# Optimization experiments

Measured on AMD Instinct MI355X. Metric: run time of the kernel, lower is better.

The kernel has to match this reference:

```python
import jax, jax.numpy as jnp
import numpy as np

N_T, N_C, N_I = 200000, 100000, 100000  # target / card / ip node counts
E = 300000                               # edges per relation
D, H, OUT = 128, 128, 2                  # embedding_size=in_size, hidden_size, out_size
# etype order: 0 card->target, 1 target->card, 2 ip->target, 3 target->ip


def setup_inputs() -> dict:
    key = jax.random.key(0)
    ks = jax.random.split(key, 14)
    return {
        "x_target": jax.random.normal(ks[0], (N_T, D), jnp.float32),
        "x_card": jax.random.normal(ks[1], (N_C, D), jnp.float32),
        "x_ip": jax.random.normal(ks[2], (N_I, D), jnp.float32),
        "w1": jax.random.normal(ks[3], (4, D, H), jnp.float32) / np.sqrt(D).astype(np.float32),
        "b1": jnp.zeros((4, H), jnp.float32),
        "w2": jax.random.normal(ks[4], (4, H, H), jnp.float32) / np.sqrt(H).astype(np.float32),
        "b2": jnp.zeros((4, H), jnp.float32),
        "w_out": jax.random.normal(ks[5], (H, OUT), jnp.float32) / np.sqrt(H).astype(np.float32),
        "b_out": jnp.zeros((OUT,), jnp.float32),
        "src0": jax.random.randint(ks[6], (E,), 0, N_C, jnp.int32),
        "dst0": jax.random.randint(ks[7], (E,), 0, N_T, jnp.int32),
        "src1": jax.random.randint(ks[8], (E,), 0, N_T, jnp.int32),
        "dst1": jax.random.randint(ks[9], (E,), 0, N_C, jnp.int32),
        "src2": jax.random.randint(ks[10], (E,), 0, N_I, jnp.int32),
        "dst2": jax.random.randint(ks[11], (E,), 0, N_T, jnp.int32),
        "src3": jax.random.randint(ks[12], (E,), 0, N_T, jnp.int32),
        "dst3": jax.random.randint(ks[13], (E,), 0, N_I, jnp.int32),
    }


def _mean_agg(msgs, dst, num_dst):
    # copy_u + mean reduce: segment-sum of gathered messages / in-degree (0 if no edges)
    s = jax.ops.segment_sum(msgs, dst, num_segments=num_dst)
    deg = jax.ops.segment_sum(jnp.ones((msgs.shape[0],), msgs.dtype), dst, num_segments=num_dst)
    return s / jnp.maximum(deg, 1.0)[:, None]


def _hetero_layer(feats, W, B, edges):
    # per-etype Linear on src feats, copy_u/mean per relation, sum across relations per dsttype
    out = {}
    for i, (src, dst, st, dt, nd) in enumerate(edges):
        Wh = feats[st] @ W[i] + B[i]          # [N_src, H] dense GEMM per etype
        agg = _mean_agg(Wh[src], dst, nd)      # gather + segment-mean (irregular)
        out[dt] = agg if dt not in out else out[dt] + agg
    return out


def reference(x_target, x_card, x_ip, w1, b1, w2, b2, w_out, b_out,
              src0, dst0, src1, dst1, src2, dst2, src3, dst3):
    edges = [
        (src0, dst0, "card", "target", N_T),
        (src1, dst1, "target", "card", N_C),
        (src2, dst2, "ip", "target", N_T),
        (src3, dst3, "target", "ip", N_I),
    ]
    h = {"target": x_target, "card": x_card, "ip": x_ip}
    h = _hetero_layer(h, w1, b1, edges)
    h = {k: jax.nn.leaky_relu(v) for k, v in h.items()}  # applied before layer i>0
    h = _hetero_layer(h, w2, b2, edges)
    logits = h["target"] @ w_out + b_out
    return jax.nn.softmax(logits, axis=-1)
```

## Files before the change

### kernel.cpp

```cpp
#include <hip/hip_runtime.h>


#define NT 200000
#define NCARD 100000
#define NIP 100000
#define NE 300000

typedef __attribute__((ext_vector_type(8))) short s8v;
typedef __attribute__((ext_vector_type(4))) float f4v;

__device__ __forceinline__ unsigned short f2b(float f) {
  unsigned u = __float_as_uint(f);
  u = (u + 0x7fff + ((u >> 16) & 1)) >> 16;
  return (unsigned short)u;
}


__global__ void hist4_k(const int* __restrict__ d1, const int* __restrict__ d3,
                        const int* __restrict__ d0, const int* __restrict__ d2,
                        int* __restrict__ g1, int* __restrict__ g3,
                        int* __restrict__ g0, int* __restrict__ g2) {
  int t = blockIdx.x * 256 + threadIdx.x;
  if (t < NE) atomicAdd(&g1[d1[t]], 1);
  else if (t < 2 * NE) atomicAdd(&g3[d3[t - NE]], 1);
  else if (t < 3 * NE) atomicAdd(&g0[d0[t - 2 * NE]], 1);
  else if (t < 4 * NE) atomicAdd(&g2[d2[t - 3 * NE]], 1);
}


__global__ void scan1f_k(const int* __restrict__ deg1, int* __restrict__ off1,
                         int* __restrict__ bs1, int nb1, int N1,
                         const int* __restrict__ deg3, int* __restrict__ off3,
                         int* __restrict__ bs3, int N3) {
  __shared__ int s[256];
  int bid = blockIdx.x;
  const int* deg; int* off; int* bsum; int N; int lb;
  if (bid < nb1) { deg = deg1; off = off1; bsum = bs1; N = N1; lb = bid; }
  else { deg = deg3; off = off3; bsum = bs3; N = N3; lb = bid - nb1; }
  int tid = threadIdx.x;
  int i = lb * 256 + tid;
  int v = (i < N) ? deg[i] : 0;
  s[tid] = v;
  __syncthreads();
  for (int o = 1; o < 256; o <<= 1) {
    int t = (tid >= o) ? s[tid - o] : 0;
    __syncthreads();
    s[tid] += t;
    __syncthreads();
  }
  if (i < N) off[i] = s[tid] - v;
  if (tid == 255) bsum[lb] = s[255];
}

__global__ void scan2f_k(int* __restrict__ bs1, int nb1, int* __restrict__ bs3, int nb3) {
  __shared__ int s[1024];
  int* bs = blockIdx.x == 0 ? bs1 : bs3;
  int nb = blockIdx.x == 0 ? nb1 : nb3;
  int t = threadIdx.x;
  int v = (t < nb) ? bs[t] : 0;
  s[t] = v;
  __syncthreads();
  for (int o = 1; o < 1024; o <<= 1) {
    int u = (t >= o) ? s[t - o] : 0;
    __syncthreads();
    s[t] += u;
    __syncthreads();
  }
  if (t < nb) bs[t] = s[t] - v;
}

__global__ void scan3f_k(int* __restrict__ off1, const int* __restrict__ bs1,
                         int* __restrict__ cur1, int nb1, int N1,
                         int* __restrict__ off3, const int* __restrict__ bs3,
                         int* __restrict__ cur3, int N3) {
  int bid = blockIdx.x;
  int* off; const int* bsum; int* cur; int N; int lb;
  if (bid < nb1) { off = off1; bsum = bs1; cur = cur1; N = N1; lb = bid; }
  else { off = off3; bsum = bs3; cur = cur3; N = N3; lb = bid - nb1; }
  int i = lb * 256 + threadIdx.x;
  if (i < N) {
    int v = off[i] + bsum[lb];
    off[i] = v;
    cur[i] = v;
  }
}

__global__ void fillf_k(const int* __restrict__ s1, const int* __restrict__ d1,
                        int* __restrict__ cur1, int* __restrict__ csr1,
                        const int* __restrict__ s3, const int* __restrict__ d3,
                        int* __restrict__ cur3, int* __restrict__ csr3) {
  int t = blockIdx.x * 256 + threadIdx.x;
  if (t < NE) {
    int slot = atomicAdd(&cur1[d1[t]], 1);
    csr1[slot] = s1[t];
  } else if (t < 2 * NE) {
    int e = t - NE;
    int slot = atomicAdd(&cur3[d3[e]], 1);
    csr3[slot] = s3[e];
  }
}


__global__ void cvt_k(const float* __restrict__ x, unsigned short* __restrict__ xb) {
  long i = (long)blockIdx.x * 256 + threadIdx.x;
  const long n4 = (long)NT * 128 / 4;
  if (i >= n4) return;
  float4 v = ((const float4*)x)[i];
  uint2 o;
  o.x = (unsigned)f2b(v.x) | ((unsigned)f2b(v.y) << 16);
  o.y = (unsigned)f2b(v.z) | ((unsigned)f2b(v.w) << 16);
  ((uint2*)xb)[i] = o;
}


__global__ void wt_k(const float* __restrict__ w1, unsigned short* __restrict__ wtC,
                     unsigned short* __restrict__ wtI) {
  int t = blockIdx.x * 256 + threadIdx.x;
  int r = t >> 14;
  int n = (t >> 7) & 127, k = t & 127;
  const float* src = w1 + (r ? 3 : 1) * 16384;
  unsigned short* dst = r ? wtI : wtC;
  dst[n * 128 + k] = f2b(src[k * 128 + n]);
}


__global__ void prep_k(const float* __restrict__ w2, const float* __restrict__ b2,
                       const float* __restrict__ wout, float* __restrict__ wfC,
                       float* __restrict__ wfI, float* __restrict__ bfC,
                       float* __restrict__ bfI) {
  int t = threadIdx.x;
  int k = t >> 1, o = t & 1;
  float sC = 0.f, sI = 0.f;
  for (int j = 0; j < 128; j++) {
    float wo = wout[j * 2 + o];
    sC += w2[0 * 16384 + k * 128 + j] * wo;
    sI += w2[2 * 16384 + k * 128 + j] * wo;
  }
  wfC[k * 2 + o] = sC;
  wfI[k * 2 + o] = sI;
  if (t < 2) {
    float s = 0.f;
    for (int j = 0; j < 128; j++) s += b2[0 * 128 + j] * wout[j * 2 + t];
    bfC[t] = s;
  } else if (t < 4) {
    int oo = t - 2;
    float s = 0.f;
    for (int j = 0; j < 128; j++) s += b2[2 * 128 + j] * wout[j * 2 + oo];
    bfI[oo] = s;
  }
}


__global__ void aggf_k(const unsigned short* __restrict__ xb,
                       const int* __restrict__ off1, const int* __restrict__ deg1,
                       const int* __restrict__ csr1, unsigned short* __restrict__ accC,
                       const int* __restrict__ off3, const int* __restrict__ deg3,
                       const int* __restrict__ csr3, unsigned short* __restrict__ accI) {
  int gt = blockIdx.x * 256 + threadIdx.x;
  int rid = gt >> 4, lane = gt & 15;
  if (rid >= NCARD + NIP) return;
  const int* off; const int* deg; const int* csr; unsigned short* acc; int row;
  if (rid < NCARD) { off = off1; deg = deg1; csr = csr1; acc = accC; row = rid; }
  else { off = off3; deg = deg3; csr = csr3; acc = accI; row = rid - NCARD; }
  int start = off[row], cnt = deg[row];
  float a[8] = {0.f, 0.f, 0.f, 0.f, 0.f, 0.f, 0.f, 0.f};
  int i = 0;
  for (; i + 2 <= cnt; i += 2) {
    int s0 = csr[start + i], s1 = csr[start + i + 1];
    uint4 v0 = *(const uint4*)(xb + (size_t)s0 * 128 + lane * 8);
    uint4 v1 = *(const uint4*)(xb + (size_t)s1 * 128 + lane * 8);
    unsigned w[8] = {v0.x, v0.y, v0.z, v0.w, v1.x, v1.y, v1.z, v1.w};
#pragma unroll
    for (int j = 0; j < 8; j++) {
      a[(j & 3) * 2] += __uint_as_float(w[j] << 16);
      a[(j & 3) * 2 + 1] += __uint_as_float(w[j] & 0xffff0000u);
    }
  }
  if (i < cnt) {
    int s0 = csr[start + i];
    uint4 v0 = *(const uint4*)(xb + (size_t)s0 * 128 + lane * 8);
    unsigned w[4] = {v0.x, v0.y, v0.z, v0.w};
#pragma unroll
    for (int j = 0; j < 4; j++) {
      a[j * 2] += __uint_as_float(w[j] << 16);
      a[j * 2 + 1] += __uint_as_float(w[j] & 0xffff0000u);
    }
  }
  uint4 o;
  o.x = (unsigned)f2b(a[0]) | ((unsigned)f2b(a[1]) << 16);
  o.y = (unsigned)f2b(a[2]) | ((unsigned)f2b(a[3]) << 16);
  o.z = (unsigned)f2b(a[4]) | ((unsigned)f2b(a[5]) << 16);
  o.w = (unsigned)f2b(a[6]) | ((unsigned)f2b(a[7]) << 16);
  *(uint4*)(acc + (size_t)row * 128 + lane * 8) = o;
}


__global__ __launch_bounds__(256) void gemm_mfma_k(
    const unsigned short* __restrict__ accC, const unsigned short* __restrict__ accI,
    const unsigned short* __restrict__ wtC, const unsigned short* __restrict__ wtI,
    const float* __restrict__ b1, const int* __restrict__ deg1,
    const int* __restrict__ deg3, const float* __restrict__ wfC,
    const float* __restrict__ wfI, const float* __restrict__ bfC,
    const float* __restrict__ bfI, float* __restrict__ zc, float* __restrict__ zi,
    int gbC) {
  int bid = blockIdx.x;
  const unsigned short* accb; const unsigned short* wt; const float* bias;
  const int* deg; const float* wf; const float* bf; float* zout; int M; int lb;
  if (bid < gbC) {
    accb = accC; wt = wtC; bias = b1 + 128; deg = deg1;
    wf = wfC; bf = bfC; zout = zc; M = NCARD; lb = bid;
  } else {
    accb = accI; wt = wtI; bias = b1 + 384; deg = deg3;
    wf = wfI; bf = bfI; zout = zi; M = NIP; lb = bid - gbC;
  }
  int wave = threadIdx.x >> 6, lane = threadIdx.x & 63;
  int q = lane >> 4, cl = lane & 15;
  int r0w = lb * 128 + wave * 32;

  s8v af[2][4];
#pragma unroll
  for (int rt = 0; rt < 2; rt++)
#pragma unroll
    for (int ks = 0; ks < 4; ks++)
      af[rt][ks] = *(const s8v*)(accb + (size_t)(r0w + rt * 16 + cl) * 128 + ks * 32 + q * 8);

  f4v acc[2][8];
#pragma unroll
  for (int rt = 0; rt < 2; rt++)
#pragma unroll
    for (int nt = 0; nt < 8; nt++) acc[rt][nt] = (f4v){0.f, 0.f, 0.f, 0.f};

#pragma unroll
  for (int nt = 0; nt < 8; nt++) {
#pragma unroll
    for (int ks = 0; ks < 4; ks++) {
      s8v bfr = *(const s8v*)(wt + (size_t)(nt * 16 + cl) * 128 + ks * 32 + q * 8);
      acc[0][nt] = __builtin_amdgcn_mfma_f32_16x16x32_bf16(af[0][ks], bfr, acc[0][nt], 0, 0, 0);
      acc[1][nt] = __builtin_amdgcn_mfma_f32_16x16x32_bf16(af[1][ks], bfr, acc[1][nt], 0, 0, 0);
    }
  }

  float2 wfv[8];
  float b1v[8];
#pragma unroll
  for (int nt = 0; nt < 8; nt++) {
    wfv[nt] = ((const float2*)wf)[nt * 16 + cl];
    b1v[nt] = bias[nt * 16 + cl];
  }
  float2 bf2 = *(const float2*)bf;
#pragma unroll
  for (int rt = 0; rt < 2; rt++) {
#pragma unroll
    for (int reg = 0; reg < 4; reg++) {
      int row = r0w + rt * 16 + q * 4 + reg;
      int d = (row < M) ? deg[row] : 0;
      float sc = (d > 0) ? 1.f / (float)d : 0.f;
      float p0 = 0.f, p1 = 0.f;
#pragma unroll
      for (int nt = 0; nt < 8; nt++) {
        float h = 0.f;
        if (d > 0) {
          h = acc[rt][nt][reg] * sc + b1v[nt];
          h = h > 0.f ? h : 0.01f * h;
        }
        p0 += h * wfv[nt].x;
        p1 += h * wfv[nt].y;
      }
#pragma unroll
      for (int o = 1; o < 16; o <<= 1) {
        p0 += __shfl_xor(p0, o);
        p1 += __shfl_xor(p1, o);
      }
      if (cl == 0 && row < M) {
        ((float2*)zout)[row] = make_float2(p0 + bf2.x, p1 + bf2.y);
      }
    }
  }
}


__global__ void scatterf_k(const int* __restrict__ s0, const int* __restrict__ d0,
                           const float* __restrict__ zc, float* __restrict__ tsum0,
                           const int* __restrict__ s2, const int* __restrict__ d2,
                           const float* __restrict__ zi, float* __restrict__ tsum2) {
  int t = blockIdx.x * 256 + threadIdx.x;
  if (t < NE) {
    float2 z = ((const float2*)zc)[s0[t]];
    int d = d0[t];
    atomicAdd(&tsum0[d * 2], z.x);
    atomicAdd(&tsum0[d * 2 + 1], z.y);
  } else if (t < 2 * NE) {
    int e = t - NE;
    float2 z = ((const float2*)zi)[s2[e]];
    int d = d2[e];
    atomicAdd(&tsum2[d * 2], z.x);
    atomicAdd(&tsum2[d * 2 + 1], z.y);
  }
}


__global__ void final3_k(const float* __restrict__ tsum0, const int* __restrict__ deg0,
                         const float* __restrict__ tsum2, const int* __restrict__ deg2,
                         const float* __restrict__ bout, float* __restrict__ out) {
  int t = blockIdx.x * 256 + threadIdx.x;
  if (t >= NT) return;
  float l0 = bout[0], l1 = bout[1];
  int d0 = deg0[t];
  if (d0 > 0) {
    float inv = 1.f / (float)d0;
    l0 += tsum0[t * 2] * inv;
    l1 += tsum0[t * 2 + 1] * inv;
  }
  int d2 = deg2[t];
  if (d2 > 0) {
    float inv = 1.f / (float)d2;
    l0 += tsum2[t * 2] * inv;
    l1 += tsum2[t * 2 + 1] * inv;
  }
  float m = fmaxf(l0, l1);
  float e0 = expf(l0 - m), e1 = expf(l1 - m);
  float inv = 1.f / (e0 + e1);
  ((float2*)out)[t] = make_float2(e0 * inv, e1 * inv);
}


extern "C" void kernel_launch(void* const* d_in, const int* in_sizes, int n_in,
                              void* d_out, int out_size, void* d_ws, size_t ws_size,
                              hipStream_t stream) {
  const float* x_target = (const float*)d_in[0];
  const float* w1 = (const float*)d_in[3];
  const float* b1 = (const float*)d_in[4];
  const float* w2 = (const float*)d_in[5];
  const float* b2 = (const float*)d_in[6];
  const float* wout = (const float*)d_in[7];
  const float* bout = (const float*)d_in[8];
  const int* src0 = (const int*)d_in[9];
  const int* dst0 = (const int*)d_in[10];
  const int* src1 = (const int*)d_in[11];
  const int* dst1 = (const int*)d_in[12];
  const int* src2 = (const int*)d_in[13];
  const int* dst2 = (const int*)d_in[14];
  const int* src3 = (const int*)d_in[15];
  const int* dst3 = (const int*)d_in[16];
  float* out = (float*)d_out;

  char* p = (char*)d_ws;
  auto alloc = [&](size_t bytes) -> char* {
    char* r = p;
    p += (bytes + 255) & ~(size_t)255;
    return r;
  };
  int* deg1 = (int*)alloc(NCARD * 4);
  int* cur1 = (int*)alloc(NCARD * 4);
  int* deg3 = (int*)alloc(NIP * 4);
  int* cur3 = (int*)alloc(NIP * 4);
  int* deg0 = (int*)alloc(NT * 4);
  int* deg2 = (int*)alloc(NT * 4);
  float* tsum0 = (float*)alloc((size_t)NT * 2 * 4);
  float* tsum2 = (float*)alloc((size_t)NT * 2 * 4);
  size_t zero_bytes = (size_t)(p - (char*)d_ws);
  int* off1 = (int*)alloc(NCARD * 4);
  int* off3 = (int*)alloc(NIP * 4);
  int* bs1 = (int*)alloc(1024 * 4);
  int* bs3 = (int*)alloc(1024 * 4);
  int* csr1 = (int*)alloc(NE * 4);
  int* csr3 = (int*)alloc(NE * 4);
  unsigned short* xb = (unsigned short*)alloc((size_t)NT * 128 * 2);
  unsigned short* accC = (unsigned short*)alloc((size_t)NCARD * 128 * 2);
  unsigned short* accI = (unsigned short*)alloc((size_t)NIP * 128 * 2);
  alloc(128 * 128 * 2);
  unsigned short* wtC = (unsigned short*)alloc(16384 * 2);
  unsigned short* wtI = (unsigned short*)alloc(16384 * 2);
  float* zc = (float*)alloc((size_t)NCARD * 2 * 4);
  float* zi = (float*)alloc((size_t)NIP * 2 * 4);
  float* wfC = (float*)alloc(256 * 4);
  float* wfI = (float*)alloc(256 * 4);
  float* bfC = (float*)alloc(2 * 4);
  float* bfI = (float*)alloc(2 * 4);

  hipMemsetAsync(d_ws, 0, zero_bytes, stream);

  hist4_k<<<(4 * NE + 255) / 256, 256, 0, stream>>>(dst1, dst3, dst0, dst2,
                                                    deg1, deg3, deg0, deg2);
  int nb1 = (NCARD + 255) / 256, nb3 = (NIP + 255) / 256;
  scan1f_k<<<nb1 + nb3, 256, 0, stream>>>(deg1, off1, bs1, nb1, NCARD,
                                          deg3, off3, bs3, NIP);
  scan2f_k<<<2, 1024, 0, stream>>>(bs1, nb1, bs3, nb3);
  scan3f_k<<<nb1 + nb3, 256, 0, stream>>>(off1, bs1, cur1, nb1, NCARD,
                                          off3, bs3, cur3, NIP);
  fillf_k<<<(2 * NE + 255) / 256, 256, 0, stream>>>(src1, dst1, cur1, csr1,
                                                    src3, dst3, cur3, csr3);

  cvt_k<<<(int)(((long)NT * 128 / 4 + 255) / 256), 256, 0, stream>>>(x_target, xb);
  wt_k<<<128, 256, 0, stream>>>(w1, wtC, wtI);
  prep_k<<<1, 256, 0, stream>>>(w2, b2, wout, wfC, wfI, bfC, bfI);

  aggf_k<<<(NCARD + NIP) / 16, 256, 0, stream>>>(xb, off1, deg1, csr1, accC,
                                                 off3, deg3, csr3, accI);

  int gbC = (NCARD + 127) / 128, gbI = (NIP + 127) / 128;
  gemm_mfma_k<<<gbC + gbI, 256, 0, stream>>>(accC, accI, wtC, wtI, b1, deg1, deg3,
                                             wfC, wfI, bfC, bfI, zc, zi, gbC);

  scatterf_k<<<(2 * NE + 255) / 256, 256, 0, stream>>>(src0, dst0, zc, tsum0,
                                                       src2, dst2, zi, tsum2);

  final3_k<<<(NT + 255) / 256, 256, 0, stream>>>(tsum0, deg0, tsum2, deg2, bout, out);
}
```

Measured before the change: 469.2 us.

## Fuse front kernels, build CSR via histogram ranks, and replace float atomics with gather

Merges histogram, weight transpose, weight fold and bf16 conversion into one launch. The histogram now records each edge's atomic rank, so the CSR fill no longer needs a second atomic pass or cursor arrays. CSR is also built for the two relations into target, so the final kernel gathers and averages per destination instead of scatter-adding floats atomically. The aggregation kernel uses one wavefront per row with four edge groups and a shuffle reduction. In exchange it adds rank-array traffic, extra scan work for two more relations, and per-thread serial loops in the final kernel.

```diff
diff --git a/kernel.cpp b/kernel.cpp
--- a/kernel.cpp
+++ b/kernel.cpp
@@ -16,27 +16,86 @@
 }
 
 
-__global__ void hist4_k(const int* __restrict__ d1, const int* __restrict__ d3,
+#define NB_HIST 4688
+#define NB_WT 128
+#define NB_CVT 25000
+
+__global__ void front_k(const float* __restrict__ x, const float* __restrict__ w1,
+                        const float* __restrict__ w2, const float* __restrict__ b2,
+                        const float* __restrict__ wout,
+                        const int* __restrict__ d1, const int* __restrict__ d3,
                         const int* __restrict__ d0, const int* __restrict__ d2,
-                        int* __restrict__ g1, int* __restrict__ g3,
-                        int* __restrict__ g0, int* __restrict__ g2) {
-  int t = blockIdx.x * 256 + threadIdx.x;
-  if (t < NE) atomicAdd(&g1[d1[t]], 1);
-  else if (t < 2 * NE) atomicAdd(&g3[d3[t - NE]], 1);
-  else if (t < 3 * NE) atomicAdd(&g0[d0[t - 2 * NE]], 1);
-  else if (t < 4 * NE) atomicAdd(&g2[d2[t - 3 * NE]], 1);
-}
-
-
-__global__ void scan1f_k(const int* __restrict__ deg1, int* __restrict__ off1,
-                         int* __restrict__ bs1, int nb1, int N1,
+                        int* __restrict__ deg1, int* __restrict__ deg3,
+                        int* __restrict__ deg0, int* __restrict__ deg2,
+                        int* __restrict__ rk1, int* __restrict__ rk3,
+                        int* __restrict__ rk0, int* __restrict__ rk2,
+                        unsigned short* __restrict__ xb, unsigned short* __restrict__ wtC,
+                        unsigned short* __restrict__ wtI, float* __restrict__ wfC,
+                        float* __restrict__ wfI, float* __restrict__ bfC,
+                        float* __restrict__ bfI) {
+  int bid = blockIdx.x, tid = threadIdx.x;
+  if (bid < NB_HIST) {
+    int t = bid * 256 + tid;
+    if (t < NE) rk1[t] = atomicAdd(&deg1[d1[t]], 1);
+    else if (t < 2 * NE) { int e = t - NE; rk3[e] = atomicAdd(&deg3[d3[e]], 1); }
+    else if (t < 3 * NE) { int e = t - 2 * NE; rk0[e] = atomicAdd(&deg0[d0[e]], 1); }
+    else if (t < 4 * NE) { int e = t - 3 * NE; rk2[e] = atomicAdd(&deg2[d2[e]], 1); }
+  } else if (bid < NB_HIST + NB_WT) {
+    int t = (bid - NB_HIST) * 256 + tid;
+    int r = t >> 14;
+    int n = (t >> 7) & 127, k = t & 127;
+    const float* src = w1 + (r ? 3 : 1) * 16384;
+    unsigned short* dst = r ? wtI : wtC;
+    dst[n * 128 + k] = f2b(src[k * 128 + n]);
+  } else if (bid == NB_HIST + NB_WT) {
+    int k = tid >> 1, o = tid & 1;
+    float sC = 0.f, sI = 0.f;
+    for (int j = 0; j < 128; j++) {
+      float wo = wout[j * 2 + o];
+      sC += w2[0 * 16384 + k * 128 + j] * wo;
+      sI += w2[2 * 16384 + k * 128 + j] * wo;
+    }
+    wfC[k * 2 + o] = sC;
+    wfI[k * 2 + o] = sI;
+    if (tid < 2) {
+      float s = 0.f;
+      for (int j = 0; j < 128; j++) s += b2[0 * 128 + j] * wout[j * 2 + tid];
+      bfC[tid] = s;
+    } else if (tid < 4) {
+      int oo = tid - 2;
+      float s = 0.f;
+      for (int j = 0; j < 128; j++) s += b2[2 * 128 + j] * wout[j * 2 + oo];
+      bfI[oo] = s;
+    }
+  } else {
+    long i = (long)(bid - (NB_HIST + NB_WT + 1)) * 256 + tid;
+    const long n4 = (long)NT * 128 / 4;
+    if (i < n4) {
+      float4 v = ((const float4*)x)[i];
+      uint2 o;
+      o.x = (unsigned)f2b(v.x) | ((unsigned)f2b(v.y) << 16);
+      o.y = (unsigned)f2b(v.z) | ((unsigned)f2b(v.w) << 16);
+      ((uint2*)xb)[i] = o;
+    }
+  }
+}
+
+
+__global__ void scan1q_k(const int* __restrict__ deg1, int* __restrict__ off1,
+                         int* __restrict__ bs1, int nb1,
                          const int* __restrict__ deg3, int* __restrict__ off3,
-                         int* __restrict__ bs3, int N3) {
+                         int* __restrict__ bs3, int nb3,
+                         const int* __restrict__ deg0, int* __restrict__ off0,
+                         int* __restrict__ bs0, int nb0,
+                         const int* __restrict__ deg2, int* __restrict__ off2,
+                         int* __restrict__ bs2) {
   __shared__ int s[256];
   int bid = blockIdx.x;
   const int* deg; int* off; int* bsum; int N; int lb;
-  if (bid < nb1) { deg = deg1; off = off1; bsum = bs1; N = N1; lb = bid; }
-  else { deg = deg3; off = off3; bsum = bs3; N = N3; lb = bid - nb1; }
+  if (bid < nb1) { deg = deg1; off = off1; bsum = bs1; N = NCARD; lb = bid; }
+  else if (bid < nb1 + nb3) { deg = deg3; off = off3; bsum = bs3; N = NIP; lb = bid - nb1; }
+  else if (bid < nb1 + nb3 + nb0) { deg = deg0; off = off0; bsum = bs0; N = NT; lb = bid - nb1 - nb3; }
+  else { deg = deg2; off = off2; bsum = bs2; N = NT; lb = bid - nb1 - nb3 - nb0; }
   int tid = threadIdx.x;
   int i = lb * 256 + tid;
   int v = (i < N) ? deg[i] : 0;
@@ -52,10 +111,14 @@
   if (tid == 255) bsum[lb] = s[255];
 }
 
-__global__ void scan2f_k(int* __restrict__ bs1, int nb1, int* __restrict__ bs3, int nb3) {
+__global__ void scan2q_k(int* __restrict__ bs1, int nb1, int* __restrict__ bs3, int nb3,
+                         int* __restrict__ bs0, int nb0, int* __restrict__ bs2, int nb2) {
   __shared__ int s[1024];
-  int* bs = blockIdx.x == 0 ? bs1 : bs3;
-  int nb = blockIdx.x == 0 ? nb1 : nb3;
+  int* bs; int nb;
+  if (blockIdx.x == 0) { bs = bs1; nb = nb1; }
+  else if (blockIdx.x == 1) { bs = bs3; nb = nb3; }
+  else if (blockIdx.x == 2) { bs = bs0; nb = nb0; }
+  else { bs = bs2; nb = nb2; }
   int t = threadIdx.x;
   int v = (t < nb) ? bs[t] : 0;
   s[t] = v;
@@ -69,85 +132,38 @@
   if (t < nb) bs[t] = s[t] - v;
 }
 
-__global__ void scan3f_k(int* __restrict__ off1, const int* __restrict__ bs1,
-                         int* __restrict__ cur1, int nb1, int N1,
-                         int* __restrict__ off3, const int* __restrict__ bs3,
-                         int* __restrict__ cur3, int N3) {
+__global__ void scan3q_k(int* __restrict__ off1, const int* __restrict__ bs1, int nb1,
+                         int* __restrict__ off3, const int* __restrict__ bs3, int nb3,
+                         int* __restrict__ off0, const int* __restrict__ bs0, int nb0,
+                         int* __restrict__ off2, const int* __restrict__ bs2) {
   int bid = blockIdx.x;
-  int* off; const int* bsum; int* cur; int N; int lb;
-  if (bid < nb1) { off = off1; bsum = bs1; cur = cur1; N = N1; lb = bid; }
-  else { off = off3; bsum = bs3; cur = cur3; N = N3; lb = bid - nb1; }
+  int* off; const int* bsum; int N; int lb;
+  if (bid < nb1) { off = off1; bsum = bs1; N = NCARD; lb = bid; }
+  else if (bid < nb1 + nb3) { off = off3; bsum = bs3; N = NIP; lb = bid - nb1; }
+  else if (bid < nb1 + nb3 + nb0) { off = off0; bsum = bs0; N = NT; lb = bid - nb1 - nb3; }
+  else { off = off2; bsum = bs2; N = NT; lb = bid - nb1 - nb3 - nb0; }
   int i = lb * 256 + threadIdx.x;
-  if (i < N) {
-    int v = off[i] + bsum[lb];
-    off[i] = v;
-    cur[i] = v;
-  }
-}
-
-__global__ void fillf_k(const int* __restrict__ s1, const int* __restrict__ d1,
-                        int* __restrict__ cur1, int* __restrict__ csr1,
+  if (i < N) off[i] += bsum[lb];
+}
+
+
+__global__ void fill4_k(const int* __restrict__ s1, const int* __restrict__ d1,
+                        const int* __restrict__ rk1, const int* __restrict__ off1,
+                        int* __restrict__ csr1,
                         const int* __restrict__ s3, const int* __restrict__ d3,
-                        int* __restrict__ cur3, int* __restrict__ csr3) {
+                        const int* __restrict__ rk3, const int* __restrict__ off3,
+                        int* __restrict__ csr3,
+                        const int* __restrict__ s0, const int* __restrict__ d0,
+                        const int* __restrict__ rk0, const int* __restrict__ off0,
+                        int* __restrict__ csr0,
+                        const int* __restrict__ s2, const int* __restrict__ d2,
+                        const int* __restrict__ rk2, const int* __restrict__ off2,
+                        int* __restrict__ csr2) {
   int t = blockIdx.x * 256 + threadIdx.x;
-  if (t < NE) {
-    int slot = atomicAdd(&cur1[d1[t]], 1);
-    csr1[slot] = s1[t];
-  } else if (t < 2 * NE) {
-    int e = t - NE;
-    int slot = atomicAdd(&cur3[d3[e]], 1);
-    csr3[slot] = s3[e];
-  }
-}
-
-
-__global__ void cvt_k(const float* __restrict__ x, unsigned short* __restrict__ xb) {
-  long i = (long)blockIdx.x * 256 + threadIdx.x;
-  const long n4 = (long)NT * 128 / 4;
-  if (i >= n4) return;
-  float4 v = ((const float4*)x)[i];
-  uint2 o;
-  o.x = (unsigned)f2b(v.x) | ((unsigned)f2b(v.y) << 16);
-  o.y = (unsigned)f2b(v.z) | ((unsigned)f2b(v.w) << 16);
-  ((uint2*)xb)[i] = o;
-}
-
-
-__global__ void wt_k(const float* __restrict__ w1, unsigned short* __restrict__ wtC,
-                     unsigned short* __restrict__ wtI) {
-  int t = blockIdx.x * 256 + threadIdx.x;
-  int r = t >> 14;
-  int n = (t >> 7) & 127, k = t & 127;
-  const float* src = w1 + (r ? 3 : 1) * 16384;
-  unsigned short* dst = r ? wtI : wtC;
-  dst[n * 128 + k] = f2b(src[k * 128 + n]);
-}
-
-
-__global__ void prep_k(const float* __restrict__ w2, const float* __restrict__ b2,
-                       const float* __restrict__ wout, float* __restrict__ wfC,
-                       float* __restrict__ wfI, float* __restrict__ bfC,
-                       float* __restrict__ bfI) {
-  int t = threadIdx.x;
-  int k = t >> 1, o = t & 1;
-  float sC = 0.f, sI = 0.f;
-  for (int j = 0; j < 128; j++) {
-    float wo = wout[j * 2 + o];
-    sC += w2[0 * 16384 + k * 128 + j] * wo;
-    sI += w2[2 * 16384 + k * 128 + j] * wo;
-  }
-  wfC[k * 2 + o] = sC;
-  wfI[k * 2 + o] = sI;
-  if (t < 2) {
-    float s = 0.f;
-    for (int j = 0; j < 128; j++) s += b2[0 * 128 + j] * wout[j * 2 + t];
-    bfC[t] = s;
-  } else if (t < 4) {
-    int oo = t - 2;
-    float s = 0.f;
-    for (int j = 0; j < 128; j++) s += b2[2 * 128 + j] * wout[j * 2 + oo];
-    bfI[oo] = s;
-  }
+  if (t < NE) csr1[off1[d1[t]] + rk1[t]] = s1[t];
+  else if (t < 2 * NE) { int e = t - NE; csr3[off3[d3[e]] + rk3[e]] = s3[e]; }
+  else if (t < 3 * NE) { int e = t - 2 * NE; csr0[off0[d0[e]] + rk0[e]] = s0[e]; }
+  else if (t < 4 * NE) { int e = t - 3 * NE; csr2[off2[d2[e]] + rk2[e]] = s2[e]; }
 }
 
 
@@ -156,42 +172,40 @@
                        const int* __restrict__ csr1, unsigned short* __restrict__ accC,
                        const int* __restrict__ off3, const int* __restrict__ deg3,
                        const int* __restrict__ csr3, unsigned short* __restrict__ accI) {
-  int gt = blockIdx.x * 256 + threadIdx.x;
-  int rid = gt >> 4, lane = gt & 15;
-  if (rid >= NCARD + NIP) return;
+  int w = (blockIdx.x * 256 + threadIdx.x) >> 6;
+  int lane = threadIdx.x & 63;
+  if (w >= NCARD + NIP) return;
   const int* off; const int* deg; const int* csr; unsigned short* acc; int row;
-  if (rid < NCARD) { off = off1; deg = deg1; csr = csr1; acc = accC; row = rid; }
-  else { off = off3; deg = deg3; csr = csr3; acc = accI; row = rid - NCARD; }
+  if (w < NCARD) { off = off1; deg = deg1; csr = csr1; acc = accC; row = w; }
+  else { off = off3; deg = deg3; csr = csr3; acc = accI; row = w - NCARD; }
   int start = off[row], cnt = deg[row];
+  int eg = lane >> 4, fl = lane & 15;
   float a[8] = {0.f, 0.f, 0.f, 0.f, 0.f, 0.f, 0.f, 0.f};
-  int i = 0;
-  for (; i + 2 <= cnt; i += 2) {
-    int s0 = csr[start + i], s1 = csr[start + i + 1];
-    uint4 v0 = *(const uint4*)(xb + (size_t)s0 * 128 + lane * 8);
-    uint4 v1 = *(const uint4*)(xb + (size_t)s1 * 128 + lane * 8);
-    unsigned w[8] = {v0.x, v0.y, v0.z, v0.w, v1.x, v1.y, v1.z, v1.w};
-#pragma unroll
-    for (int j = 0; j < 8; j++) {
-      a[(j & 3) * 2] += __uint_as_float(w[j] << 16);
-      a[(j & 3) * 2 + 1] += __uint_as_float(w[j] & 0xffff0000u);
-    }
-  }
-  if (i < cnt) {
-    int s0 = csr[start + i];
-    uint4 v0 = *(const uint4*)(xb + (size_t)s0 * 128 + lane * 8);
-    unsigned w[4] = {v0.x, v0.y, v0.z, v0.w};
-#pragma unroll
-    for (int j = 0; j < 4; j++) {
-      a[j * 2] += __uint_as_float(w[j] << 16);
-      a[j * 2 + 1] += __uint_as_float(w[j] & 0xffff0000u);
-    }
-  }
-  uint4 o;
-  o.x = (unsigned)f2b(a[0]) | ((unsigned)f2b(a[1]) << 16);
-  o.y = (unsigned)f2b(a[2]) | ((unsigned)f2b(a[3]) << 16);
-  o.z = (unsigned)f2b(a[4]) | ((unsigned)f2b(a[5]) << 16);
-  o.w = (unsigned)f2b(a[6]) | ((unsigned)f2b(a[7]) << 16);
-  *(uint4*)(acc + (size_t)row * 128 + lane * 8) = o;
+  for (int i = eg; i < cnt; i += 4) {
+    int s = csr[start + i];
+    uint4 v = *(const uint4*)(xb + (size_t)s * 128 + fl * 8);
+    a[0] += __uint_as_float(v.x << 16);
+    a[1] += __uint_as_float(v.x & 0xffff0000u);
+    a[2] += __uint_as_float(v.y << 16);
+    a[3] += __uint_as_float(v.y & 0xffff0000u);
+    a[4] += __uint_as_float(v.z << 16);
+    a[5] += __uint_as_float(v.z & 0xffff0000u);
+    a[6] += __uint_as_float(v.w << 16);
+    a[7] += __uint_as_float(v.w & 0xffff0000u);
+  }
+#pragma unroll
+  for (int j = 0; j < 8; j++) {
+    a[j] += __shfl_xor(a[j], 16);
+    a[j] += __shfl_xor(a[j], 32);
+  }
+  if (eg == 0) {
+    uint4 o;
+    o.x = (unsigned)f2b(a[0]) | ((unsigned)f2b(a[1]) << 16);
+    o.y = (unsigned)f2b(a[2]) | ((unsigned)f2b(a[3]) << 16);
+    o.z = (unsigned)f2b(a[4]) | ((unsigned)f2b(a[5]) << 16);
+    o.w = (unsigned)f2b(a[6]) | ((unsigned)f2b(a[7]) << 16);
+    *(uint4*)(acc + (size_t)row * 128 + fl * 8) = o;
+  }
 }
 
 
@@ -279,43 +293,37 @@
 }
 
 
-__global__ void scatterf_k(const int* __restrict__ s0, const int* __restrict__ d0,
-                           const float* __restrict__ zc, float* __restrict__ tsum0,
-                           const int* __restrict__ s2, const int* __restrict__ d2,
-                           const float* __restrict__ zi, float* __restrict__ tsum2) {
-  int t = blockIdx.x * 256 + threadIdx.x;
-  if (t < NE) {
-    float2 z = ((const float2*)zc)[s0[t]];
-    int d = d0[t];
-    atomicAdd(&tsum0[d * 2], z.x);
-    atomicAdd(&tsum0[d * 2 + 1], z.y);
-  } else if (t < 2 * NE) {
-    int e = t - NE;
-    float2 z = ((const float2*)zi)[s2[e]];
-    int d = d2[e];
-    atomicAdd(&tsum2[d * 2], z.x);
-    atomicAdd(&tsum2[d * 2 + 1], z.y);
-  }
-}
-
-
-__global__ void final3_k(const float* __restrict__ tsum0, const int* __restrict__ deg0,
-                         const float* __restrict__ tsum2, const int* __restrict__ deg2,
+__global__ void finalg_k(const float* __restrict__ zc, const float* __restrict__ zi,
+                         const int* __restrict__ off0, const int* __restrict__ deg0,
+                         const int* __restrict__ csr0, const int* __restrict__ off2,
+                         const int* __restrict__ deg2, const int* __restrict__ csr2,
                          const float* __restrict__ bout, float* __restrict__ out) {
   int t = blockIdx.x * 256 + threadIdx.x;
   if (t >= NT) return;
   float l0 = bout[0], l1 = bout[1];
-  int d0 = deg0[t];
-  if (d0 > 0) {
-    float inv = 1.f / (float)d0;
-    l0 += tsum0[t * 2] * inv;
-    l1 += tsum0[t * 2 + 1] * inv;
-  }
-  int d2 = deg2[t];
-  if (d2 > 0) {
-    float inv = 1.f / (float)d2;
-    l0 += tsum2[t * 2] * inv;
-    l1 += tsum2[t * 2 + 1] * inv;
+  {
+    int d = deg0[t], st = off0[t];
+    if (d > 0) {
+      float ax = 0.f, ay = 0.f;
+      for (int i = 0; i < d; i++) {
+        float2 z = ((const float2*)zc)[csr0[st + i]];
+        ax += z.x; ay += z.y;
+      }
+      float inv = 1.f / (float)d;
+      l0 += ax * inv; l1 += ay * inv;
+    }
+  }
+  {
+    int d = deg2[t], st = off2[t];
+    if (d > 0) {
+      float ax = 0.f, ay = 0.f;
+      for (int i = 0; i < d; i++) {
+        float2 z = ((const float2*)zi)[csr2[st + i]];
+        ax += z.x; ay += z.y;
+      }
+      float inv = 1.f / (float)d;
+      l0 += ax * inv; l1 += ay * inv;
+    }
   }
   float m = fmaxf(l0, l1);
   float e0 = expf(l0 - m), e1 = expf(l1 - m);
@@ -351,20 +359,26 @@
     return r;
   };
   int* deg1 = (int*)alloc(NCARD * 4);
-  int* cur1 = (int*)alloc(NCARD * 4);
   int* deg3 = (int*)alloc(NIP * 4);
-  int* cur3 = (int*)alloc(NIP * 4);
   int* deg0 = (int*)alloc(NT * 4);
   int* deg2 = (int*)alloc(NT * 4);
-  float* tsum0 = (float*)alloc((size_t)NT * 2 * 4);
-  float* tsum2 = (float*)alloc((size_t)NT * 2 * 4);
   size_t zero_bytes = (size_t)(p - (char*)d_ws);
+  int* rk1 = (int*)alloc(NE * 4);
+  int* rk3 = (int*)alloc(NE * 4);
+  int* rk0 = (int*)alloc(NE * 4);
+  int* rk2 = (int*)alloc(NE * 4);
   int* off1 = (int*)alloc(NCARD * 4);
   int* off3 = (int*)alloc(NIP * 4);
+  int* off0 = (int*)alloc(NT * 4);
+  int* off2 = (int*)alloc(NT * 4);
   int* bs1 = (int*)alloc(1024 * 4);
   int* bs3 = (int*)alloc(1024 * 4);
+  int* bs0 = (int*)alloc(1024 * 4);
+  int* bs2 = (int*)alloc(1024 * 4);
   int* csr1 = (int*)alloc(NE * 4);
   int* csr3 = (int*)alloc(NE * 4);
+  int* csr0 = (int*)alloc(NE * 4);
+  int* csr2 = (int*)alloc(NE * 4);
   unsigned short* xb = (unsigned short*)alloc((size_t)NT * 128 * 2);
   unsigned short* accC = (unsigned short*)alloc((size_t)NCARD * 128 * 2);
   unsigned short* accI = (unsigned short*)alloc((size_t)NIP * 128 * 2);
@@ -380,30 +394,29 @@
 
   hipMemsetAsync(d_ws, 0, zero_bytes, stream);
 
-  hist4_k<<<(4 * NE + 255) / 256, 256, 0, stream>>>(dst1, dst3, dst0, dst2,
-                                                    deg1, deg3, deg0, deg2);
+  front_k<<<NB_HIST + NB_WT + 1 + NB_CVT, 256, 0, stream>>>(
+      x_target, w1, w2, b2, wout, dst1, dst3, dst0, dst2, deg1, deg3, deg0, deg2,
+      rk1, rk3, rk0, rk2, xb, wtC, wtI, wfC, wfI, bfC, bfI);
+
   int nb1 = (NCARD + 255) / 256, nb3 = (NIP + 255) / 256;
-  scan1f_k<<<nb1 + nb3, 256, 0, stream>>>(deg1, off1, bs1, nb1, NCARD,
-                                          deg3, off3, bs3, NIP);
-  scan2f_k<<<2, 1024, 0, stream>>>(bs1, nb1, bs3, nb3);
-  scan3f_k<<<nb1 + nb3, 256, 0, stream>>>(off1, bs1, cur1, nb1, NCARD,
-                                          off3, bs3, cur3, NIP);
-  fillf_k<<<(2 * NE + 255) / 256, 256, 0, stream>>>(src1, dst1, cur1, csr1,
-                                                    src3, dst3, cur3, csr3);
-
-  cvt_k<<<(int)(((long)NT * 128 / 4 + 255) / 256), 256, 0, stream>>>(x_target, xb);
-  wt_k<<<128, 256, 0, stream>>>(w1, wtC, wtI);
-  prep_k<<<1, 256, 0, stream>>>(w2, b2, wout, wfC, wfI, bfC, bfI);
-
-  aggf_k<<<(NCARD + NIP) / 16, 256, 0, stream>>>(xb, off1, deg1, csr1, accC,
-                                                 off3, deg3, csr3, accI);
+  int nb0 = (NT + 255) / 256, nb2 = (NT + 255) / 256;
+  scan1q_k<<<nb1 + nb3 + nb0 + nb2, 256, 0, stream>>>(
+      deg1, off1, bs1, nb1, deg3, off3, bs3, nb3, deg0, off0, bs0, nb0, deg2, off2, bs2);
+  scan2q_k<<<4, 1024, 0, stream>>>(bs1, nb1, bs3, nb3, bs0, nb0, bs2, nb2);
+  scan3q_k<<<nb1 + nb3 + nb0 + nb2, 256, 0, stream>>>(
+      off1, bs1, nb1, off3, bs3, nb3, off0, bs0, nb0, off2, bs2);
+
+  fill4_k<<<(4 * NE + 255) / 256, 256, 0, stream>>>(
+      src1, dst1, rk1, off1, csr1, src3, dst3, rk3, off3, csr3,
+      src0, dst0, rk0, off0, csr0, src2, dst2, rk2, off2, csr2);
+
+  aggf_k<<<(NCARD + NIP + 3) / 4, 256, 0, stream>>>(xb, off1, deg1, csr1, accC,
+                                                    off3, deg3, csr3, accI);
 
   int gbC = (NCARD + 127) / 128, gbI = (NIP + 127) / 128;
   gemm_mfma_k<<<gbC + gbI, 256, 0, stream>>>(accC, accI, wtC, wtI, b1, deg1, deg3,
                                              wfC, wfI, bfC, bfI, zc, zi, gbC);
 
-  scatterf_k<<<(2 * NE + 255) / 256, 256, 0, stream>>>(src0, dst0, zc, tsum0,
-                                                       src2, dst2, zi, tsum2);
-
-  final3_k<<<(NT + 255) / 256, 256, 0, stream>>>(tsum0, deg0, tsum2, deg2, bout, out);
-}
+  finalg_k<<<(NT + 255) / 256, 256, 0, stream>>>(zc, zi, off0, deg0, csr0,
+                                                 off2, deg2, csr2, bout, out);
+}
```

Measured after the change: 408.9 us. -12.9%, faster.
